# Kernel tuning notes

Hardware: AMD Instinct MI355X
Metric: run time of the kernel (lower is better)

## Reference

```python
import jax, jax.numpy as jnp
import numpy as np

B, C, H, W = 16, 256, 56, 56
HEADS = 4
C_OUT = 256
K = 3
SQ = 16  # squeeze_rate (C=256 >= 80, so not halved)
BN_EPS = 1e-5


def setup_inputs() -> dict:
    key = jax.random.key(0)
    ks = jax.random.split(key, 9)
    r = C // SQ
    cper = C_OUT // HEADS
    return {
        "x": jax.random.normal(ks[0], (B, C, H, W), dtype=jnp.float32),
        "bn_gamma": 1.0 + 0.1 * jax.random.normal(ks[1], (C,), dtype=jnp.float32),
        "bn_beta": 0.1 * jax.random.normal(ks[2], (C,), dtype=jnp.float32),
        "bn_mean": 0.1 * jax.random.normal(ks[3], (C,), dtype=jnp.float32),
        "bn_var": 0.5 + jax.random.uniform(ks[4], (C,), dtype=jnp.float32),
        "fc1_w": 0.1 * jax.random.normal(ks[5], (HEADS, r, C), dtype=jnp.float32),
        "fc2_w": 0.1 * jax.random.normal(ks[6], (HEADS, C, r), dtype=jnp.float32),
        "fc2_b": jnp.ones((HEADS, C), dtype=jnp.float32),  # init.constant_(bias, 1.0)
        "conv_w": 0.05 * jax.random.normal(ks[7], (HEADS, cper, C, K, K), dtype=jnp.float32),
        "inactive_channels": 192,
    }


def reference(x, bn_gamma, bn_beta, bn_mean, bn_var, fc1_w, fc2_w, fc2_b, conv_w, inactive_channels):
    b, c, h, w = x.shape
    heads = fc1_w.shape[0]
    # BatchNorm (inference, running stats) + ReLU
    inv = jax.lax.rsqrt(bn_var + BN_EPS)
    xn = jax.nn.relu((x - bn_mean[None, :, None, None]) * (bn_gamma * inv)[None, :, None, None]
                     + bn_beta[None, :, None, None])
    # Global average pool -> [b, c]
    x_avg = xn.mean(axis=(2, 3))
    # Per-head SE gate: relu(fc2(relu(fc1(x_avg))))  -> [heads, b, c]
    y1 = jax.nn.relu(jnp.einsum("bc,hrc->hbr", x_avg, fc1_w))
    mask = jax.nn.relu(jnp.einsum("hbr,hcr->hbc", y1, fc2_w) + fc2_b[:, None, :])
    lasso_loss = mask.mean(axis=(1, 2)).sum()  # sum over heads of per-head mean
    # topk smallest -> threshold; zero out mask values <= k-th smallest (detached cmp)
    mask_d = jax.lax.stop_gradient(mask)
    if inactive_channels > 0:
        neg_vals, _ = jax.lax.top_k(-mask_d, inactive_channels)  # k largest of -mask
        thresh = -neg_vals[..., -1:]  # k-th smallest of mask, [heads, b, 1]
        mask_c = jnp.where(mask_d <= thresh, 0.0, mask)
    else:
        mask_c = mask
    # Apply per-head channel mask and stack heads: [b, heads*c, h, w]
    mc = jnp.transpose(mask_c, (1, 0, 2))  # [b, heads, c]
    x_mask = (xn[:, None, :, :, :] * mc[:, :, :, None, None]).reshape(b, heads * c, h, w)
    # Grouped conv (groups=heads), weight [heads*cper, c, K, K]
    wflat = conv_w.reshape(-1, c, K, K)
    out = jax.lax.conv_general_dilated(
        x_mask, wflat, window_strides=(1, 1), padding=[(1, 1), (1, 1)],
        dimension_numbers=("NCHW", "OIHW", "NCHW"), feature_group_count=heads)
    bo, co, ho, wo = out.shape
    out = out.reshape(bo, heads, co // heads, ho, wo).transpose(0, 2, 1, 3, 4).reshape(bo, co, ho, wo)
    return out, lasso_loss
```

## Files before the change

kernel.cpp:

```cpp
#include <hip/hip_runtime.h>
#include <hip/hip_bf16.h>
#include <math.h>

#define B_     16
#define C_     256
#define H_     56
#define W_     56
#define HEADS_ 4
#define CPER_  64
#define R_     16
#define HW_    (H_*W_)
#define BN_EPS_ 1e-5f

typedef short bf16x8 __attribute__((ext_vector_type(8)));
typedef float f32x4  __attribute__((ext_vector_type(4)));

__device__ inline unsigned short f2bf(float f) {
    unsigned int u = __builtin_bit_cast(unsigned int, f);
    u += 0x7fffu + ((u >> 16) & 1u);
    return (unsigned short)(u >> 16);
}

__global__ __launch_bounds__(64) void k_pool(
    const float* __restrict__ x,
    const float* __restrict__ gamma, const float* __restrict__ beta,
    const float* __restrict__ mean,  const float* __restrict__ var,
    float* __restrict__ xavg)
{
    int plane = blockIdx.x;
    int c = plane & (C_ - 1);
    float s = gamma[c] * rsqrtf(var[c] + BN_EPS_);
    float t = fmaf(-mean[c], s, beta[c]);
    const float4* xp = (const float4*)(x + (size_t)plane * HW_);
    float sum = 0.f;
    for (int i = threadIdx.x; i < HW_ / 4; i += 64) {
        float4 v = xp[i];
        sum += fmaxf(fmaf(v.x, s, t), 0.f) + fmaxf(fmaf(v.y, s, t), 0.f)
             + fmaxf(fmaf(v.z, s, t), 0.f) + fmaxf(fmaf(v.w, s, t), 0.f);
    }
    for (int off = 32; off; off >>= 1) sum += __shfl_down(sum, off, 64);
    if (threadIdx.x == 0) xavg[plane] = sum * (1.f / HW_);
}

__global__ __launch_bounds__(256) void k_wt2(const float* __restrict__ w,
                                             float* __restrict__ wt2f)
{
    int i = blockIdx.x * 256 + threadIdx.x;
    if (i >= HEADS_ * 9 * CPER_ * C_) return;
    int c = i & 255, j = (i >> 8) & 63, ht = i >> 14;
    int h = ht / 9, t = ht - h * 9;
    wt2f[i] = w[((size_t)((h * CPER_ + j) * C_ + c)) * 9 + t];
}

__global__ __launch_bounds__(256) void k_se(
    const float* __restrict__ xavg,
    const float* __restrict__ fc1, const float* __restrict__ fc2,
    const float* __restrict__ fc2b, const int* __restrict__ kptr,
    float* __restrict__ maskc, int* __restrict__ aidx64,
    int* __restrict__ act_cnt, float* __restrict__ lasso)
{
    int hb = blockIdx.x;
    int h = hb / B_, b = hb - h * B_;
    int tid = threadIdx.x;

    __shared__ float sav[C_], sy1[R_], smask[C_], sred[4], sthr;
    __shared__ int scnt, s_ord[C_];

    sav[tid] = xavg[b * C_ + tid];
    if (tid == 0) scnt = 0;
    __syncthreads();

    if (tid < R_) {
        const float* w = fc1 + (size_t)(h * R_ + tid) * C_;
        float acc = 0.f;
        for (int c2 = 0; c2 < C_; ++c2) acc = fmaf(sav[c2], w[c2], acc);
        sy1[tid] = fmaxf(acc, 0.f);
    }
    __syncthreads();

    const float* w2 = fc2 + (size_t)(h * C_ + tid) * R_;
    float acc = fc2b[h * C_ + tid];
    for (int r = 0; r < R_; ++r) acc = fmaf(sy1[r], w2[r], acc);
    float m = fmaxf(acc, 0.f);
    smask[tid] = m;
    __syncthreads();

    float ls = m;
    for (int off = 32; off > 0; off >>= 1) ls += __shfl_down(ls, off, 64);
    int lane = tid & 63, wv = tid >> 6;
    if (lane == 0) sred[wv] = ls;

    int cl = 0, ce = 0;
    for (int j = 0; j < C_; ++j) {
        float vj = smask[j];
        cl += (vj < m);
        ce += (vj == m);
    }
    if (tid == 0) sthr = -1e30f;
    __syncthreads();
    int k = kptr[0];
    if (k > 0 && cl <= k - 1 && (k - 1) < cl + ce) sthr = m;
    __syncthreads();

    float thr = sthr;
    float mc = (m <= thr) ? 0.f : m;
    maskc[hb * C_ + tid] = mc;
    if (mc != 0.f) {
        int p = atomicAdd(&scnt, 1);
        s_ord[p] = tid;
    }
    __syncthreads();
    if (tid < 64) aidx64[hb * 64 + tid] = (tid < scnt) ? s_ord[tid] : 0;
    if (tid == 0) {
        act_cnt[hb] = scnt;
        atomicAdd(lasso, (sred[0] + sred[1] + sred[2] + sred[3]) * (1.f / (B_ * C_)));
    }
}

__global__ __launch_bounds__(256) void k_wgather(
    const float* __restrict__ wt2f, const float* __restrict__ maskc,
    const int* __restrict__ aidx64, const int* __restrict__ acnt,
    short* __restrict__ Wc)
{
    int t = blockIdx.x, hb = blockIdx.y;
    int h = hb >> 4;
    int tid = threadIdx.x;
    int cnt = acnt[hb];
    __shared__ int s_act[64];
    __shared__ float s_mv[64];
    if (tid < 64) {
        int a = aidx64[hb * 64 + tid];
        s_act[tid] = a;
        s_mv[tid]  = (tid < cnt) ? maskc[hb * C_ + a] : 0.f;
    }
    __syncthreads();
    const float* wsrc = wt2f + (size_t)(h * 9 + t) * (CPER_ * C_);
    short* wdst = Wc + (size_t)(hb * 9 + t) * (CPER_ * 64);
    for (int it = 0; it < 16; ++it) {
        int e = it * 256 + tid;
        int cp = e & 63, j = e >> 6;
        float v = wsrc[j * C_ + s_act[cp]] * s_mv[cp];
        int slot = (cp + 8 * (j & 7)) & 63;
        wdst[j * 64 + slot] = (short)f2bf(v);
    }
}

__global__ __launch_bounds__(256) void k_bnc(
    const float* __restrict__ x,
    const float* __restrict__ gamma, const float* __restrict__ beta,
    const float* __restrict__ mean,  const float* __restrict__ var,
    const int* __restrict__ aidx64, short* __restrict__ xc)
{
    int y = blockIdx.x, b = blockIdx.y;
    int tid = threadIdx.x;
    __shared__ unsigned short T[W_ * 258];
    __shared__ float ss[C_], st[C_];
    __shared__ short sact[256];

    {
        float s = gamma[tid] * rsqrtf(var[tid] + BN_EPS_);
        ss[tid] = s;
        st[tid] = fmaf(-mean[tid], s, beta[tid]);
        int h = tid >> 6, cp = tid & 63;
        sact[tid] = (short)aidx64[(h * B_ + b) * 64 + cp];
    }
    __syncthreads();

    const float* xrow = x + (size_t)b * C_ * HW_ + y * W_;
    for (int i = tid; i < C_ * 14; i += 256) {
        int c = i / 14, f = i - c * 14;
        float4 v = *(const float4*)(xrow + (size_t)c * HW_ + f * 4);
        float s = ss[c], t = st[c];
        int xb = f * 4;
        T[(xb + 0) * 258 + c] = f2bf(fmaxf(fmaf(v.x, s, t), 0.f));
        T[(xb + 1) * 258 + c] = f2bf(fmaxf(fmaf(v.y, s, t), 0.f));
        T[(xb + 2) * 258 + c] = f2bf(fmaxf(fmaf(v.z, s, t), 0.f));
        T[(xb + 3) * 258 + c] = f2bf(fmaxf(fmaf(v.w, s, t), 0.f));
    }
    __syncthreads();

    unsigned int* ob = (unsigned int*)xc;
    #pragma unroll
    for (int h = 0; h < HEADS_; ++h) {
        size_t obase = ((size_t)(h * B_ + b) * HW_ + (size_t)y * W_) * 32;
        for (int i = tid; i < W_ * 32; i += 256) {
            int px = i >> 5, d = i & 31;
            unsigned int lo = T[px * 258 + sact[h * 64 + 2 * d]];
            unsigned int hi = T[px * 258 + sact[h * 64 + 2 * d + 1]];
            ob[obase + i] = lo | (hi << 16);
        }
    }
}

__global__ __launch_bounds__(256, 3) void k_conv(
    const short* __restrict__ xc, const short* __restrict__ Wc,
    float* __restrict__ out)
{
    int g = blockIdx.x;
    int vx = g & 7, r = g >> 3;
    int hb = vx * 8 + r / 14;
    int band = r - (r / 14) * 14;
    int h = hb >> 4, b = hb & 15;
    int tid = threadIdx.x, lane = tid & 63, wv = tid >> 6;
    int y0 = band * 4;
    int m = lane & 15, q = lane >> 4;

    __shared__ short sW[2][4096];

    const short* Wh = Wc + (size_t)hb * 9 * 4096;
    const short* xb = xc + (size_t)hb * HW_ * 64;
    int soff = wv * 512 + lane * 8;

    {
        bf16x8 w0 = *(const bf16x8*)(Wh + soff);
        bf16x8 w1 = *(const bf16x8*)(Wh + 2048 + soff);
        *(bf16x8*)&sW[0][soff] = w0;
        *(bf16x8*)&sW[0][2048 + soff] = w1;
    }
    __syncthreads();

    f32x4 acc[4][4];
    #pragma unroll
    for (int i = 0; i < 4; ++i)
        #pragma unroll
        for (int j = 0; j < 4; ++j)
            #pragma unroll
            for (int rr = 0; rr < 4; ++rr) acc[i][j][rr] = 0.f;

    int yrow = y0 + wv;
    int arot = q * 8 + 8 * (m & 7);

    #pragma unroll
    for (int t = 0; t < 9; ++t) {
        const int dy = t / 3 - 1, dx = t % 3 - 1;
        bf16x8 w0, w1;
        if (t < 8) {
            const short* Wn = Wh + (t + 1) * 4096;
            w0 = *(const bf16x8*)(Wn + soff);
            w1 = *(const bf16x8*)(Wn + 2048 + soff);
        }
        int gy = yrow + dy;
        bool gyok = (unsigned)gy < (unsigned)H_;
        const short* sWc = sW[t & 1];

        #pragma unroll
        for (int c0 = 0; c0 < 64; c0 += 32) {
            bf16x8 aF[4], bF[4];
            #pragma unroll
            for (int jt = 0; jt < 4; ++jt)
                aF[jt] = *(const bf16x8*)&sWc[(jt * 16 + m) * 64 + ((c0 + arot) & 63)];
            #pragma unroll
            for (int xt = 0; xt < 4; ++xt) {
                int gx = xt * 16 + m + dx;
                bf16x8 v = {0, 0, 0, 0, 0, 0, 0, 0};
                if (gyok && (unsigned)gx < (unsigned)W_)
                    v = *(const bf16x8*)(xb + ((size_t)(gy * W_ + gx)) * 64 + c0 + q * 8);
                bF[xt] = v;
            }
            #pragma unroll
            for (int jt = 0; jt < 4; ++jt)
                #pragma unroll
                for (int xt = 0; xt < 4; ++xt)
                    acc[jt][xt] = __builtin_amdgcn_mfma_f32_16x16x32_bf16(
                        aF[jt], bF[xt], acc[jt][xt], 0, 0, 0);
        }
        if (t < 8) {
            *(bf16x8*)&sW[(t + 1) & 1][soff] = w0;
            *(bf16x8*)&sW[(t + 1) & 1][2048 + soff] = w1;
        }
        __syncthreads();
    }

    #pragma unroll
    for (int xt = 0; xt < 4; ++xt) {
        int xx = xt * 16 + m;
        if (xx < W_) {
            #pragma unroll
            for (int jt = 0; jt < 4; ++jt)
                #pragma unroll
                for (int rr = 0; rr < 4; ++rr) {
                    int j = jt * 16 + q * 4 + rr;
                    int oc = j * HEADS_ + h;
                    out[(((size_t)b * C_ + oc) * H_ + yrow) * W_ + xx] = acc[jt][xt][rr];
                }
        }
    }
}

extern "C" void kernel_launch(void* const* d_in, const int* in_sizes, int n_in,
                              void* d_out, int out_size, void* d_ws, size_t ws_size,
                              hipStream_t stream)
{
    const float* x     = (const float*)d_in[0];
    const float* gamma = (const float*)d_in[1];
    const float* beta  = (const float*)d_in[2];
    const float* mean  = (const float*)d_in[3];
    const float* var   = (const float*)d_in[4];
    const float* fc1   = (const float*)d_in[5];
    const float* fc2   = (const float*)d_in[6];
    const float* fc2b  = (const float*)d_in[7];
    const float* convw = (const float*)d_in[8];
    const int*   kptr  = (const int*)d_in[9];

    float* out   = (float*)d_out;
    float* lasso = out + (size_t)B_ * C_ * HW_;

    char* ws = (char*)d_ws;
    size_t off = 0;
    short* xc    = (short*)(ws + off); off += (size_t)HEADS_ * B_ * HW_ * 64 * 2;
    off = (off + 255) & ~(size_t)255;
    float* xavg  = (float*)(ws + off); off += (size_t)B_ * C_ * 4;
    float* maskc = (float*)(ws + off); off += (size_t)HEADS_ * B_ * C_ * 4;
    int*   aidx64= (int*)  (ws + off); off += (size_t)HEADS_ * B_ * 64 * 4;
    int*   acnt  = (int*)  (ws + off); off += (size_t)HEADS_ * B_ * 4;
    off = (off + 255) & ~(size_t)255;
    float* wt2f  = (float*)(ws + off); off += (size_t)HEADS_ * 9 * CPER_ * C_ * 4;
    off = (off + 255) & ~(size_t)255;
    short* Wc    = (short*)(ws + off); off += (size_t)HEADS_ * B_ * 9 * CPER_ * 64 * 2;

    hipMemsetAsync(lasso, 0, 4, stream);

    k_wt2<<<(HEADS_ * 9 * CPER_ * C_ + 255) / 256, 256, 0, stream>>>(convw, wt2f);
    k_pool<<<B_ * C_, 64, 0, stream>>>(x, gamma, beta, mean, var, xavg);
    k_se<<<HEADS_ * B_, 256, 0, stream>>>(xavg, fc1, fc2, fc2b, kptr,
                                          maskc, aidx64, acnt, lasso);
    k_wgather<<<dim3(9, HEADS_ * B_), 256, 0, stream>>>(wt2f, maskc, aidx64, acnt, Wc);
    k_bnc<<<dim3(H_, B_), 256, 0, stream>>>(x, gamma, beta, mean, var, aidx64, xc);
    k_conv<<<HEADS_ * B_ * (H_ / 4), 256, 0, stream>>>(xc, Wc, out);
}
```

Measured before the change: 194.3 us.

## Fuse BN into pool pass, pad conv input, and drop LDS weight staging

The pooling kernel now also writes a bf16 BN+ReLU copy of x. The gather kernel reads that half-size buffer for only the active channels instead of re-reading all fp32 channels. The conv input is stored with a zero halo so the conv needs no bounds checks, and the weight transpose kernel is removed by reading conv weights directly in the gather. The conv kernel loads A and B fragments straight from global memory into registers, software-pipelined across channel halves, instead of double-buffering weights through LDS with barriers. The cost is an extra bf16 intermediate write and strided weight reads, plus possible uncoalesced gathers.

After: 224.8 us. +15.7%, slower.

```diff
diff --git a/kernel.cpp b/kernel.cpp
--- a/kernel.cpp
+++ b/kernel.cpp
@@ -11,6 +11,7 @@
 #define R_     16
 #define HW_    (H_*W_)
 #define BN_EPS_ 1e-5f
+#define XPAD   58
 
 typedef short bf16x8 __attribute__((ext_vector_type(8)));
 typedef float f32x4  __attribute__((ext_vector_type(4)));
@@ -20,36 +21,40 @@
     u += 0x7fffu + ((u >> 16) & 1u);
     return (unsigned short)(u >> 16);
 }
-
-__global__ __launch_bounds__(64) void k_pool(
+__device__ inline unsigned int pack2(float a, float b) {
+    return (unsigned int)f2bf(a) | ((unsigned int)f2bf(b) << 16);
+}
+
+__global__ __launch_bounds__(256) void k_bn(
     const float* __restrict__ x,
     const float* __restrict__ gamma, const float* __restrict__ beta,
     const float* __restrict__ mean,  const float* __restrict__ var,
-    float* __restrict__ xavg)
+    unsigned int* __restrict__ xnb, float* __restrict__ xavg)
 {
     int plane = blockIdx.x;
     int c = plane & (C_ - 1);
+    int tid = threadIdx.x;
     float s = gamma[c] * rsqrtf(var[c] + BN_EPS_);
     float t = fmaf(-mean[c], s, beta[c]);
     const float4* xp = (const float4*)(x + (size_t)plane * HW_);
+    uint2* xo = (uint2*)(xnb + (size_t)plane * (HW_ / 2));
     float sum = 0.f;
-    for (int i = threadIdx.x; i < HW_ / 4; i += 64) {
+    for (int i = tid; i < HW_ / 4; i += 256) {
         float4 v = xp[i];
-        sum += fmaxf(fmaf(v.x, s, t), 0.f) + fmaxf(fmaf(v.y, s, t), 0.f)
-             + fmaxf(fmaf(v.z, s, t), 0.f) + fmaxf(fmaf(v.w, s, t), 0.f);
+        float a0 = fmaxf(fmaf(v.x, s, t), 0.f);
+        float a1 = fmaxf(fmaf(v.y, s, t), 0.f);
+        float a2 = fmaxf(fmaf(v.z, s, t), 0.f);
+        float a3 = fmaxf(fmaf(v.w, s, t), 0.f);
+        sum += a0 + a1 + a2 + a3;
+        uint2 o; o.x = pack2(a0, a1); o.y = pack2(a2, a3);
+        xo[i] = o;
     }
     for (int off = 32; off; off >>= 1) sum += __shfl_down(sum, off, 64);
-    if (threadIdx.x == 0) xavg[plane] = sum * (1.f / HW_);
-}
-
-__global__ __launch_bounds__(256) void k_wt2(const float* __restrict__ w,
-                                             float* __restrict__ wt2f)
-{
-    int i = blockIdx.x * 256 + threadIdx.x;
-    if (i >= HEADS_ * 9 * CPER_ * C_) return;
-    int c = i & 255, j = (i >> 8) & 63, ht = i >> 14;
-    int h = ht / 9, t = ht - h * 9;
-    wt2f[i] = w[((size_t)((h * CPER_ + j) * C_ + c)) * 9 + t];
+    __shared__ float sred[4];
+    int lane = tid & 63, wv = tid >> 6;
+    if (lane == 0) sred[wv] = sum;
+    __syncthreads();
+    if (tid == 0) xavg[plane] = (sred[0] + sred[1] + sred[2] + sred[3]) * (1.f / HW_);
 }
 
 __global__ __launch_bounds__(256) void k_se(
@@ -118,7 +123,7 @@
 }
 
 __global__ __launch_bounds__(256) void k_wgather(
-    const float* __restrict__ wt2f, const float* __restrict__ maskc,
+    const float* __restrict__ convw, const float* __restrict__ maskc,
     const int* __restrict__ aidx64, const int* __restrict__ acnt,
     short* __restrict__ Wc)
 {
@@ -134,63 +139,61 @@
         s_mv[tid]  = (tid < cnt) ? maskc[hb * C_ + a] : 0.f;
     }
     __syncthreads();
-    const float* wsrc = wt2f + (size_t)(h * 9 + t) * (CPER_ * C_);
     short* wdst = Wc + (size_t)(hb * 9 + t) * (CPER_ * 64);
     for (int it = 0; it < 16; ++it) {
         int e = it * 256 + tid;
         int cp = e & 63, j = e >> 6;
-        float v = wsrc[j * C_ + s_act[cp]] * s_mv[cp];
-        int slot = (cp + 8 * (j & 7)) & 63;
-        wdst[j * 64 + slot] = (short)f2bf(v);
-    }
-}
-
-__global__ __launch_bounds__(256) void k_bnc(
-    const float* __restrict__ x,
-    const float* __restrict__ gamma, const float* __restrict__ beta,
-    const float* __restrict__ mean,  const float* __restrict__ var,
-    const int* __restrict__ aidx64, short* __restrict__ xc)
-{
-    int y = blockIdx.x, b = blockIdx.y;
-    int tid = threadIdx.x;
-    __shared__ unsigned short T[W_ * 258];
-    __shared__ float ss[C_], st[C_];
-    __shared__ short sact[256];
-
-    {
-        float s = gamma[tid] * rsqrtf(var[tid] + BN_EPS_);
-        ss[tid] = s;
-        st[tid] = fmaf(-mean[tid], s, beta[tid]);
-        int h = tid >> 6, cp = tid & 63;
-        sact[tid] = (short)aidx64[(h * B_ + b) * 64 + cp];
-    }
-    __syncthreads();
-
-    const float* xrow = x + (size_t)b * C_ * HW_ + y * W_;
-    for (int i = tid; i < C_ * 14; i += 256) {
-        int c = i / 14, f = i - c * 14;
-        float4 v = *(const float4*)(xrow + (size_t)c * HW_ + f * 4);
-        float s = ss[c], t = st[c];
-        int xb = f * 4;
-        T[(xb + 0) * 258 + c] = f2bf(fmaxf(fmaf(v.x, s, t), 0.f));
-        T[(xb + 1) * 258 + c] = f2bf(fmaxf(fmaf(v.y, s, t), 0.f));
-        T[(xb + 2) * 258 + c] = f2bf(fmaxf(fmaf(v.z, s, t), 0.f));
-        T[(xb + 3) * 258 + c] = f2bf(fmaxf(fmaf(v.w, s, t), 0.f));
-    }
-    __syncthreads();
-
-    unsigned int* ob = (unsigned int*)xc;
-    #pragma unroll
-    for (int h = 0; h < HEADS_; ++h) {
-        size_t obase = ((size_t)(h * B_ + b) * HW_ + (size_t)y * W_) * 32;
-        for (int i = tid; i < W_ * 32; i += 256) {
-            int px = i >> 5, d = i & 31;
-            unsigned int lo = T[px * 258 + sact[h * 64 + 2 * d]];
-            unsigned int hi = T[px * 258 + sact[h * 64 + 2 * d + 1]];
-            ob[obase + i] = lo | (hi << 16);
-        }
-    }
-}
+        float v = convw[((size_t)((h * CPER_ + j) * C_ + s_act[cp])) * 9 + t] * s_mv[cp];
+        wdst[j * 64 + cp] = (short)f2bf(v);
+    }
+}
+
+__global__ __launch_bounds__(256) void k_bnc2(
+    const unsigned short* __restrict__ xnb, const int* __restrict__ aidx64,
+    short* __restrict__ xc)
+{
+    int y = blockIdx.x, hb = blockIdx.y;
+    int b = hb & 15;
+    int tid = threadIdx.x;
+    __shared__ unsigned short T[64 * 58];
+    __shared__ int s_act[64];
+    if (tid < 64) s_act[tid] = aidx64[hb * 64 + tid];
+    __syncthreads();
+
+    const unsigned int* xs = (const unsigned int*)xnb;
+    for (int i = tid; i < 64 * 28; i += 256) {
+        int ch = i / 28, d = i - ch * 28;
+        unsigned int v = xs[(size_t)(b * C_ + s_act[ch]) * (HW_ / 2) + y * (W_ / 2) + d];
+        *(unsigned int*)&T[ch * 58 + 2 * d] = v;
+    }
+    __syncthreads();
+
+    unsigned int* xcd = (unsigned int*)(xc + (size_t)hb * XPAD * XPAD * 64);
+    int row = (y + 1) * XPAD;
+    for (int i = tid; i < W_ * 32; i += 256) {
+        int px = i >> 5, dd = i & 31;
+        unsigned int lo = T[(2 * dd)     * 58 + px];
+        unsigned int hi = T[(2 * dd + 1) * 58 + px];
+        xcd[(size_t)(row + px + 1) * 32 + dd] = lo | (hi << 16);
+    }
+    if (tid < 64) xcd[(size_t)(row + (tid >> 5) * (XPAD - 1)) * 32 + (tid & 31)] = 0;
+    if (y == 0)      for (int i = tid; i < XPAD * 32; i += 256) xcd[i] = 0;
+    if (y == H_ - 1) for (int i = tid; i < XPAD * 32; i += 256)
+        xcd[(size_t)(XPAD - 1) * XPAD * 32 + i] = 0;
+}
+
+#define LOADA(dst, T, C0) { const short* wp_ = Wh + (T) * 4096 + m * 64 + (C0) + q * 8; \
+    _Pragma("unroll") for (int jt_ = 0; jt_ < 4; ++jt_) \
+        dst[jt_] = *(const bf16x8*)(wp_ + jt_ * 1024); }
+
+#define LOADB(dst, DY, DX, C0) { int rb_ = (yrow + (DY) + 1) * XPAD; \
+    _Pragma("unroll") for (int xt_ = 0; xt_ < 4; ++xt_) { \
+        int gx_ = xt_ * 16 + m + (DX) + 1; gx_ = gx_ > 57 ? 57 : gx_; \
+        dst[xt_] = *(const bf16x8*)(xb + (size_t)(rb_ + gx_) * 64 + (C0) + q * 8); } }
+
+#define MFMA16(A_, B_v) _Pragma("unroll") for (int jt_ = 0; jt_ < 4; ++jt_) \
+    _Pragma("unroll") for (int xt_ = 0; xt_ < 4; ++xt_) \
+        acc[jt_][xt_] = __builtin_amdgcn_mfma_f32_16x16x32_bf16(A_[jt_], B_v[xt_], acc[jt_][xt_], 0, 0, 0);
 
 __global__ __launch_bounds__(256, 3) void k_conv(
     const short* __restrict__ xc, const short* __restrict__ Wc,
@@ -202,22 +205,11 @@
     int band = r - (r / 14) * 14;
     int h = hb >> 4, b = hb & 15;
     int tid = threadIdx.x, lane = tid & 63, wv = tid >> 6;
-    int y0 = band * 4;
     int m = lane & 15, q = lane >> 4;
-
-    __shared__ short sW[2][4096];
+    int yrow = band * 4 + wv;
 
     const short* Wh = Wc + (size_t)hb * 9 * 4096;
-    const short* xb = xc + (size_t)hb * HW_ * 64;
-    int soff = wv * 512 + lane * 8;
-
-    {
-        bf16x8 w0 = *(const bf16x8*)(Wh + soff);
-        bf16x8 w1 = *(const bf16x8*)(Wh + 2048 + soff);
-        *(bf16x8*)&sW[0][soff] = w0;
-        *(bf16x8*)&sW[0][2048 + soff] = w1;
-    }
-    __syncthreads();
+    const short* xb = xc + (size_t)hb * XPAD * XPAD * 64;
 
     f32x4 acc[4][4];
     #pragma unroll
@@ -227,48 +219,23 @@
             #pragma unroll
             for (int rr = 0; rr < 4; ++rr) acc[i][j][rr] = 0.f;
 
-    int yrow = y0 + wv;
-    int arot = q * 8 + 8 * (m & 7);
-
-    #pragma unroll
+    bf16x8 Ac[4], Bc[4], An[4], Bn[4];
+    int dy = -1, dx = -1;
+    LOADA(Ac, 0, 0)
+    LOADB(Bc, dy, dx, 0)
+
     for (int t = 0; t < 9; ++t) {
-        const int dy = t / 3 - 1, dx = t % 3 - 1;
-        bf16x8 w0, w1;
+        int dxn = (dx == 1) ? -1 : dx + 1;
+        int dyn = (dx == 1) ? dy + 1 : dy;
+        LOADA(An, t, 32)
+        LOADB(Bn, dy, dx, 32)
+        MFMA16(Ac, Bc)
         if (t < 8) {
-            const short* Wn = Wh + (t + 1) * 4096;
-            w0 = *(const bf16x8*)(Wn + soff);
-            w1 = *(const bf16x8*)(Wn + 2048 + soff);
+            LOADA(Ac, (t + 1), 0)
+            LOADB(Bc, dyn, dxn, 0)
         }
-        int gy = yrow + dy;
-        bool gyok = (unsigned)gy < (unsigned)H_;
-        const short* sWc = sW[t & 1];
-
-        #pragma unroll
-        for (int c0 = 0; c0 < 64; c0 += 32) {
-            bf16x8 aF[4], bF[4];
-            #pragma unroll
-            for (int jt = 0; jt < 4; ++jt)
-                aF[jt] = *(const bf16x8*)&sWc[(jt * 16 + m) * 64 + ((c0 + arot) & 63)];
-            #pragma unroll
-            for (int xt = 0; xt < 4; ++xt) {
-                int gx = xt * 16 + m + dx;
-                bf16x8 v = {0, 0, 0, 0, 0, 0, 0, 0};
-                if (gyok && (unsigned)gx < (unsigned)W_)
-                    v = *(const bf16x8*)(xb + ((size_t)(gy * W_ + gx)) * 64 + c0 + q * 8);
-                bF[xt] = v;
-            }
-            #pragma unroll
-            for (int jt = 0; jt < 4; ++jt)
-                #pragma unroll
-                for (int xt = 0; xt < 4; ++xt)
-                    acc[jt][xt] = __builtin_amdgcn_mfma_f32_16x16x32_bf16(
-                        aF[jt], bF[xt], acc[jt][xt], 0, 0, 0);
-        }
-        if (t < 8) {
-            *(bf16x8*)&sW[(t + 1) & 1][soff] = w0;
-            *(bf16x8*)&sW[(t + 1) & 1][2048 + soff] = w1;
-        }
-        __syncthreads();
+        MFMA16(An, Bn)
+        dy = dyn; dx = dxn;
     }
 
     #pragma unroll
@@ -307,24 +274,23 @@
 
     char* ws = (char*)d_ws;
     size_t off = 0;
-    short* xc    = (short*)(ws + off); off += (size_t)HEADS_ * B_ * HW_ * 64 * 2;
+    unsigned int* xnb = (unsigned int*)(ws + off); off += (size_t)B_ * C_ * HW_ * 2;
+    off = (off + 255) & ~(size_t)255;
+    short* xc    = (short*)(ws + off); off += (size_t)HEADS_ * B_ * XPAD * XPAD * 64 * 2;
     off = (off + 255) & ~(size_t)255;
     float* xavg  = (float*)(ws + off); off += (size_t)B_ * C_ * 4;
     float* maskc = (float*)(ws + off); off += (size_t)HEADS_ * B_ * C_ * 4;
     int*   aidx64= (int*)  (ws + off); off += (size_t)HEADS_ * B_ * 64 * 4;
     int*   acnt  = (int*)  (ws + off); off += (size_t)HEADS_ * B_ * 4;
     off = (off + 255) & ~(size_t)255;
-    float* wt2f  = (float*)(ws + off); off += (size_t)HEADS_ * 9 * CPER_ * C_ * 4;
-    off = (off + 255) & ~(size_t)255;
     short* Wc    = (short*)(ws + off); off += (size_t)HEADS_ * B_ * 9 * CPER_ * 64 * 2;
 
     hipMemsetAsync(lasso, 0, 4, stream);
 
-    k_wt2<<<(HEADS_ * 9 * CPER_ * C_ + 255) / 256, 256, 0, stream>>>(convw, wt2f);
-    k_pool<<<B_ * C_, 64, 0, stream>>>(x, gamma, beta, mean, var, xavg);
+    k_bn<<<B_ * C_, 256, 0, stream>>>(x, gamma, beta, mean, var, xnb, xavg);
     k_se<<<HEADS_ * B_, 256, 0, stream>>>(xavg, fc1, fc2, fc2b, kptr,
                                           maskc, aidx64, acnt, lasso);
-    k_wgather<<<dim3(9, HEADS_ * B_), 256, 0, stream>>>(wt2f, maskc, aidx64, acnt, Wc);
-    k_bnc<<<dim3(H_, B_), 256, 0, stream>>>(x, gamma, beta, mean, var, aidx64, xc);
+    k_wgather<<<dim3(9, HEADS_ * B_), 256, 0, stream>>>(convw, maskc, aidx64, acnt, Wc);
+    k_bnc2<<<dim3(H_, HEADS_ * B_), 256, 0, stream>>>((const unsigned short*)xnb, aidx64, xc);
     k_conv<<<HEADS_ * B_ * (H_ / 4), 256, 0, stream>>>(xc, Wc, out);
 }
```
